# Kernel tuning notes

Measured on AMD Instinct MI355X. Metric: run time of the kernel, lower is better.

## Reference

```python
import jax, jax.numpy as jnp
import numpy as np

GN_EPS = 1e-5
GN_GROUPS = 8
KNN_EPS = 1e-8


def group_norm(x, w, b):
    # x: [B, C, N]
    B, C, N = x.shape
    xg = x.reshape(B, GN_GROUPS, C // GN_GROUPS, N)
    mu = jnp.mean(xg, axis=(2, 3), keepdims=True)
    var = jnp.var(xg, axis=(2, 3), keepdims=True)
    xg = (xg - mu) * jax.lax.rsqrt(var + GN_EPS)
    return xg.reshape(B, C, N) * w[None, :, None] + b[None, :, None]


def swish(x):
    return x * jax.nn.sigmoid(x)


def three_interpolate(points_coords, centers_coords, centers_features):
    # points_coords [B,3,N], centers_coords [B,3,M], centers_features [B,C,M]
    B, _, N = points_coords.shape
    C = centers_features.shape[1]
    p2 = jnp.sum(points_coords ** 2, axis=1)            # [B,N]
    c2 = jnp.sum(centers_coords ** 2, axis=1)           # [B,M]
    cross = jnp.einsum('bdn,bdm->bnm', points_coords, centers_coords)
    dist2 = p2[:, :, None] + c2[:, None, :] - 2.0 * cross  # [B,N,M] squared dists
    neg_d, idx = jax.lax.top_k(-dist2, 3)               # 3 smallest -> [B,N,3]
    d = -neg_d
    w = 1.0 / (d + KNN_EPS)
    w = w / jnp.sum(w, axis=-1, keepdims=True)          # [B,N,3]
    featsT = jnp.swapaxes(centers_features, 1, 2)       # [B,M,C]
    gathered = jnp.take_along_axis(featsT, idx.reshape(B, N * 3, 1), axis=1)
    gathered = gathered.reshape(B, N, 3, C)
    out = jnp.einsum('bnk,bnkc->bcn', w, gathered)      # [B,C,N]
    return out


def setup_inputs() -> dict:
    key = jax.random.key(0)
    ks = jax.random.split(key, 8)
    B, N, M = 8, 8192, 2048
    C_ctr, C_pts, D = 256, 128, 64
    Cin, C1, C2 = C_ctr + C_pts, 256, 256
    return {
        'points_coords': jax.random.normal(ks[0], (B, 3, N), jnp.float32),
        'centers_coords': jax.random.normal(ks[1], (B, 3, M), jnp.float32),
        'centers_features': jax.random.normal(ks[2], (B, C_ctr, M), jnp.float32),
        'points_features': jax.random.normal(ks[3], (B, C_pts, N), jnp.float32),
        'time_emb': jax.random.normal(ks[4], (B, D, 1), jnp.float32),
        'W1': jax.random.normal(ks[5], (C1, Cin), jnp.float32) * (1.0 / np.sqrt(Cin)),
        'b1': jnp.zeros((C1,), jnp.float32),
        'gn1_w': jnp.ones((C1,), jnp.float32),
        'gn1_b': jnp.zeros((C1,), jnp.float32),
        'W2': jax.random.normal(ks[6], (C2, C1), jnp.float32) * (1.0 / np.sqrt(C1)),
        'b2': jnp.zeros((C2,), jnp.float32),
        'gn2_w': jnp.ones((C2,), jnp.float32),
        'gn2_b': jnp.zeros((C2,), jnp.float32),
    }


def reference(points_coords, centers_coords, centers_features, points_features,
              time_emb, W1, b1, gn1_w, gn1_b, W2, b2, gn2_w, gn2_b):
    interp = three_interpolate(points_coords, centers_coords, centers_features)
    x = jnp.concatenate([interp, points_features], axis=1)  # [B, Cin, N]
    # SharedMLP layer 1: Conv1d(k=1) + GroupNorm(8) + Swish
    x = jnp.einsum('oc,bcn->bon', W1, x) + b1[None, :, None]
    x = swish(group_norm(x, gn1_w, gn1_b))
    # layer 2
    x = jnp.einsum('oc,bcn->bon', W2, x) + b2[None, :, None]
    x = swish(group_norm(x, gn2_w, gn2_b))
    N = points_coords.shape[-1]
    time_emb_exp = jnp.broadcast_to(time_emb[:, :, 0:1], time_emb.shape[:2] + (N,))
    return (x, points_coords, time_emb_exp)
```

## Files before the change

### kernel.cpp

```cpp
#include <hip/hip_runtime.h>
#include <hip/hip_bf16.h>
#include <float.h>

#define B_ 8
#define N_ 8192
#define M_ 2048
#define CC_ 256
#define CP_ 128
#define CIN_ 384
#define GRP_ 8

typedef __attribute__((ext_vector_type(8))) short short8;
typedef __attribute__((ext_vector_type(4))) short short4v;
typedef __attribute__((ext_vector_type(4))) float f32x4;

static __device__ __forceinline__ float bf2f(unsigned short u) {
  union { unsigned int i; float f; } v; v.i = ((unsigned int)u) << 16; return v.f;
}
static __device__ __forceinline__ unsigned short f2bf(float f) {
  union { float f; unsigned int i; } v; v.f = f;
  unsigned int u = v.i;
  unsigned int r = (u + 0x7FFFu + ((u >> 16) & 1u)) >> 16;
  return (unsigned short)r;
}
static __device__ __forceinline__ void gload16(const void* g, void* l) {
  __builtin_amdgcn_global_load_lds(
      (const __attribute__((address_space(1))) void*)g,
      (__attribute__((address_space(3))) void*)l, 16, 0, 0);
}

__global__ __launch_bounds__(512) void k_front(
    const float* __restrict__ pc, const float* __restrict__ cc,
    int* __restrict__ idx, float* __restrict__ wts,
    const float* __restrict__ W1, const float* __restrict__ W2,
    short* __restrict__ W1b, short* __restrict__ W2b,
    const float* __restrict__ cf, short* __restrict__ FT,
    const float* __restrict__ pf, short* __restrict__ x0T,
    const float* __restrict__ te, float* __restrict__ out) {
  __shared__ __align__(16) char smem[32768];
  int bid = blockIdx.x;
  int t = threadIdx.x;
  if (bid < 512) {
    float4* ctr = (float4*)smem;
    double (*mk)[3][128] = (double(*)[3][128])smem;
    int b = bid >> 6;
    int base = (bid & 63) * 128;
    const float* ccb = cc + (size_t)b * 3 * M_;
    for (int i = t; i < M_; i += 512) {
      float x = ccb[i], y = ccb[M_ + i], z = ccb[2 * M_ + i];
      ctr[i] = make_float4(x, y, z, x * x + y * y + z * z);
    }
    __syncthreads();
    int wv = t >> 6, lane = t & 63;
    const float* pcb = pc + (size_t)b * 3 * N_;
    int na = base + lane, nb = base + 64 + lane;
    float pxa = pcb[na], pya = pcb[N_ + na], pza = pcb[2 * N_ + na];
    float pxb = pcb[nb], pyb = pcb[N_ + nb], pzb = pcb[2 * N_ + nb];
    float p2a = pxa * pxa + pya * pya + pza * pza;
    float p2b = pxb * pxb + pyb * pyb + pzb * pzb;
    const double kinit = __hiloint2double(0x7F7FFFFF, 0);
    double a0 = kinit, a1 = kinit, a2 = kinit;
    double e0 = kinit, e1 = kinit, e2 = kinit;
    const float4* C = ctr + wv * 256;
    int mbase = wv * 256;
#pragma unroll 8
    for (int m = 0; m < 256; ++m) {
      float4 c = C[m];
      float dota = pxa * c.x;
      dota = __builtin_fmaf(pya, c.y, dota);
      dota = __builtin_fmaf(pza, c.z, dota);
      float da = __builtin_fmaf(-2.f, dota, c.w) + p2a;
      float dotb = pxb * c.x;
      dotb = __builtin_fmaf(pyb, c.y, dotb);
      dotb = __builtin_fmaf(pzb, c.z, dotb);
      float db = __builtin_fmaf(-2.f, dotb, c.w) + p2b;
      double ka = __hiloint2double(__float_as_int(da), mbase + m);
      double kb = __hiloint2double(__float_as_int(db), mbase + m);
      double t0 = fmin(ka, a0);
      double t1 = fmin(fmax(ka, a0), a1);
      double t2 = fmin(fmax(ka, a1), a2);
      a0 = t0; a1 = t1; a2 = t2;
      double u0 = fmin(kb, e0);
      double u1 = fmin(fmax(kb, e0), e1);
      double u2 = fmin(fmax(kb, e1), e2);
      e0 = u0; e1 = u1; e2 = u2;
    }
    __syncthreads();
    mk[wv][0][lane] = a0; mk[wv][1][lane] = a1; mk[wv][2][lane] = a2;
    mk[wv][0][64 + lane] = e0; mk[wv][1][64 + lane] = e1; mk[wv][2][64 + lane] = e2;
    __syncthreads();
    if (t < 128) {
      double k0 = kinit, k1 = kinit, k2 = kinit;
#pragma unroll
      for (int w = 0; w < 8; ++w) {
#pragma unroll
        for (int j = 0; j < 3; ++j) {
          double key = mk[w][j][t];
          double n0 = fmin(key, k0);
          double n1 = fmin(fmax(key, k0), k1);
          double n2 = fmin(fmax(key, k1), k2);
          k0 = n0; k1 = n1; k2 = n2;
        }
      }
      float d0 = __int_as_float(__double2hiint(k0));
      float d1 = __int_as_float(__double2hiint(k1));
      float d2 = __int_as_float(__double2hiint(k2));
      float w0 = 1.f / (d0 + 1e-8f), w1 = 1.f / (d1 + 1e-8f), w2 = 1.f / (d2 + 1e-8f);
      float inv = 1.f / (w0 + w1 + w2);
      int bn = b * N_ + base + t;
      wts[bn] = w0 * inv; wts[B_ * N_ + bn] = w1 * inv; wts[2 * B_ * N_ + bn] = w2 * inv;
      idx[bn] = __double2loint(k0);
      idx[B_ * N_ + bn] = __double2loint(k1);
      idx[2 * B_ * N_ + bn] = __double2loint(k2);
    }
  } else if (bid < 704) {
    int i = (bid - 512) * 512 + t;
    if (i < 256 * CIN_) W1b[i] = (short)f2bf(W1[i]);
    if (i < 256 * 256)  W2b[i] = (short)f2bf(W2[i]);
  } else if (bid < 6848) {
    int q2 = (bid - 704) * 2 + (t >> 8);
    int tt = t & 255;
    float (*tile)[33] = (float(*)[33])(smem + (t >> 8) * 4352);
    const float* in; short* outp;
    int C, Nn, RS, coff, n0, c0, b;
    if (q2 < 4096) {
      in = cf; outp = FT; C = CC_; Nn = M_; RS = CC_; coff = 0;
      n0 = (q2 & 63) * 32; c0 = ((q2 >> 6) & 7) * 32; b = q2 >> 9;
    } else {
      int q = q2 - 4096;
      in = pf; outp = x0T; C = CP_; Nn = N_; RS = CIN_; coff = 256;
      n0 = (q & 255) * 32; c0 = ((q >> 8) & 3) * 32; b = q >> 10;
    }
    const float* inb = in + (size_t)b * C * Nn;
    short* outb = outp + (size_t)b * Nn * RS;
    int tx = tt & 31, ty = tt >> 5;
#pragma unroll
    for (int i = 0; i < 32; i += 8)
      tile[ty + i][tx] = inb[(size_t)(c0 + ty + i) * Nn + n0 + tx];
    __syncthreads();
#pragma unroll
    for (int i = 0; i < 32; i += 8)
      outb[(size_t)(n0 + ty + i) * RS + coff + c0 + tx] = (short)f2bf(tile[tx][ty + i]);
  } else {
    int total = 196608 + B_ * 64 * N_;
    for (int i = (bid - 6848) * 512 + t; i < total; i += 512 * 512) {
      if (i < 196608) {
        out[16777216 + i] = pc[i];
      } else {
        int j = i - 196608;
        int bd = j >> 13;
        out[16973824 + j] = te[bd];
      }
    }
  }
}

__global__ __launch_bounds__(256) void k_interp(
    const short* __restrict__ FT, const int* __restrict__ idx,
    const float* __restrict__ wts, short* __restrict__ x0T) {
  int b = blockIdx.y;
  int t = threadIdx.x;
  int nl = t >> 5, cch = (t & 31) * 8;
  int n = blockIdx.x * 8 + nl;
  int bn = b * N_ + n;
  int i0 = idx[bn], i1 = idx[B_ * N_ + bn], i2 = idx[2 * B_ * N_ + bn];
  float w0 = wts[bn], w1 = wts[B_ * N_ + bn], w2 = wts[2 * B_ * N_ + bn];
  const short* Fb = FT + (size_t)b * M_ * CC_;
  short8 f0 = *(const short8*)(Fb + (size_t)i0 * CC_ + cch);
  short8 f1 = *(const short8*)(Fb + (size_t)i1 * CC_ + cch);
  short8 f2 = *(const short8*)(Fb + (size_t)i2 * CC_ + cch);
  short8 r;
#pragma unroll
  for (int e = 0; e < 8; ++e) {
    float v = w0 * bf2f((unsigned short)f0[e]) + w1 * bf2f((unsigned short)f1[e]) +
              w2 * bf2f((unsigned short)f2[e]);
    r[e] = (short)f2bf(v);
  }
  *(short8*)(x0T + (size_t)bn * CIN_ + cch) = r;
}

__global__ __launch_bounds__(256) void k_gemm(
    const short* __restrict__ Wb, const short* __restrict__ Xb,
    const float* __restrict__ bias, short* __restrict__ Yb,
    float* __restrict__ part, int K) {
  __shared__ __align__(16) short sW[128 * 64];
  __shared__ __align__(16) short sX[128 * 64];
  int b = blockIdx.z;
  int otile = blockIdx.x * 128;
  int ntile = blockIdx.y * 128;
  int t = threadIdx.x;
  int wv = t >> 6, lane = t & 63;
  int wr = wv >> 1, wc = wv & 1;
  int fr = lane & 15;
  int g = lane >> 4;
  f32x4 acc[4][4] = {};
  const short* Wp = Wb + (size_t)otile * K;
  const short* Xp = Xb + ((size_t)b * N_ + ntile) * K;
  for (int k0 = 0; k0 < K; k0 += 64) {
#pragma unroll
    for (int j = 0; j < 4; ++j) {
      int s = j * 256 + t;
      int row = s >> 3;
      int kc = (s & 7) ^ (row & 7);
      gload16(Wp + (size_t)row * K + k0 + kc * 8, sW + j * 2048 + wv * 512);
      gload16(Xp + (size_t)row * K + k0 + kc * 8, sX + j * 2048 + wv * 512);
    }
    __syncthreads();
#pragma unroll
    for (int h = 0; h < 2; ++h) {
      short8 af[4], bfr[4];
#pragma unroll
      for (int m = 0; m < 4; ++m) {
        int ra = wr * 64 + m * 16 + fr;
        af[m] = *(const short8*)(sW + ra * 64 + (((h * 4 + g) ^ (ra & 7)) << 3));
        int rb = wc * 64 + m * 16 + fr;
        bfr[m] = *(const short8*)(sX + rb * 64 + (((h * 4 + g) ^ (rb & 7)) << 3));
      }
#pragma unroll
      for (int m = 0; m < 4; ++m)
#pragma unroll
        for (int nn = 0; nn < 4; ++nn)
          acc[m][nn] = __builtin_amdgcn_mfma_f32_16x16x32_bf16(af[m], bfr[nn], acc[m][nn], 0, 0, 0);
    }
    __syncthreads();
  }
  float s01 = 0.f, ss01 = 0.f, s23 = 0.f, ss23 = 0.f;
#pragma unroll
  for (int m = 0; m < 4; ++m) {
    int o = otile + wr * 64 + m * 16 + g * 4;
    float4 bi = *(const float4*)(bias + o);
#pragma unroll
    for (int nn = 0; nn < 4; ++nn) {
      int n = ntile + wc * 64 + nn * 16 + fr;
      float v0 = acc[m][nn][0] + bi.x;
      float v1 = acc[m][nn][1] + bi.y;
      float v2 = acc[m][nn][2] + bi.z;
      float v3 = acc[m][nn][3] + bi.w;
      if (m < 2) { s01 += v0 + v1 + v2 + v3; ss01 += v0*v0 + v1*v1 + v2*v2 + v3*v3; }
      else       { s23 += v0 + v1 + v2 + v3; ss23 += v0*v0 + v1*v1 + v2*v2 + v3*v3; }
      short4v sv;
      sv[0] = (short)f2bf(v0);
      sv[1] = (short)f2bf(v1);
      sv[2] = (short)f2bf(v2);
      sv[3] = (short)f2bf(v3);
      *(short4v*)(Yb + ((size_t)b * N_ + n) * 256 + o) = sv;
    }
  }
#pragma unroll
  for (int off = 32; off > 0; off >>= 1) {
    s01 += __shfl_down(s01, off);
    ss01 += __shfl_down(ss01, off);
    s23 += __shfl_down(s23, off);
    ss23 += __shfl_down(ss23, off);
  }
  float* wred = (float*)sW;
  if (lane == 0) {
    wred[wv * 4 + 0] = s01; wred[wv * 4 + 1] = ss01;
    wred[wv * 4 + 2] = s23; wred[wv * 4 + 3] = ss23;
  }
  __syncthreads();
  if (t < 8) {
    int gl = t >> 1, sel = t & 1;
    int wrn = gl >> 1;
    int id = (gl & 1) * 2 + sel;
    float v = wred[(wrn * 2 + 0) * 4 + id] + wred[(wrn * 2 + 1) * 4 + id];
    part[(((size_t)b * 8 + blockIdx.x * 4 + gl) * 64 + blockIdx.y) * 2 + sel] = v;
  }
}

__global__ __launch_bounds__(256) void k_gnapply(short* __restrict__ Y,
                                                 const float* __restrict__ part,
                                                 const float* __restrict__ gw,
                                                 const float* __restrict__ gb) {
  __shared__ float fs[128];
  int t = threadIdx.x;
  if (t < 64) {
    float s = 0.f, ss = 0.f;
    for (int j = 0; j < 64; ++j) {
      s += part[((size_t)t * 64 + j) * 2];
      ss += part[((size_t)t * 64 + j) * 2 + 1];
    }
    const float cnt = 32.f * 8192.f;
    float mean = s / cnt;
    float var = ss / cnt - mean * mean;
    fs[t * 2] = mean;
    fs[t * 2 + 1] = rsqrtf(var + 1e-5f);
  }
  __syncthreads();
  unsigned int* Yd = (unsigned int*)Y;
  int total = B_ * N_ * 128;
  for (int i = blockIdx.x * blockDim.x + t; i < total;
       i += gridDim.x * blockDim.x) {
    int o2 = i & 127;
    int b = i >> 20;
    int g = o2 >> 4;
    float mean = fs[(b * 8 + g) * 2], rstd = fs[(b * 8 + g) * 2 + 1];
    unsigned int v = Yd[i];
    int o = o2 * 2;
    float a = bf2f((unsigned short)(v & 0xFFFF));
    float c = bf2f((unsigned short)(v >> 16));
    a = (a - mean) * rstd * gw[o] + gb[o];
    c = (c - mean) * rstd * gw[o + 1] + gb[o + 1];
    a = a / (1.f + __expf(-a));
    c = c / (1.f + __expf(-c));
    Yd[i] = (unsigned int)f2bf(a) | ((unsigned int)f2bf(c) << 16);
  }
}

__global__ __launch_bounds__(256) void k_gnapply_out(
    const short* __restrict__ Y, const float* __restrict__ part,
    const float* __restrict__ gw, const float* __restrict__ gb,
    float* __restrict__ out) {
  __shared__ float tile[64][65];
  __shared__ float fs[16];
  int b = blockIdx.z;
  int t = threadIdx.x;
  if (t < 8) {
    float s = 0.f, ss = 0.f;
    for (int j = 0; j < 64; ++j) {
      s += part[(((size_t)b * 8 + t) * 64 + j) * 2];
      ss += part[(((size_t)b * 8 + t) * 64 + j) * 2 + 1];
    }
    const float cnt = 32.f * 8192.f;
    float mean = s / cnt;
    float var = ss / cnt - mean * mean;
    fs[t * 2] = mean;
    fs[t * 2 + 1] = rsqrtf(var + 1e-5f);
  }
  __syncthreads();
  int n0 = blockIdx.x * 64, o0 = blockIdx.y * 64;
  int row = t >> 5, dcol = t & 31;
  const unsigned int* Yd = (const unsigned int*)(Y + (size_t)b * N_ * 256);
  int o = o0 + dcol * 2;
  int g = o >> 5;
  float mean = fs[g * 2], rstd = fs[g * 2 + 1];
  float w0 = gw[o], w1 = gw[o + 1], bb0 = gb[o], bb1 = gb[o + 1];
#pragma unroll
  for (int p = 0; p < 8; ++p) {
    int n = n0 + p * 8 + row;
    unsigned int v = Yd[(size_t)n * 128 + (o0 >> 1) + dcol];
    float a = bf2f((unsigned short)(v & 0xFFFF));
    float c = bf2f((unsigned short)(v >> 16));
    a = (a - mean) * rstd * w0 + bb0; a = a / (1.f + __expf(-a));
    c = (c - mean) * rstd * w1 + bb1; c = c / (1.f + __expf(-c));
    tile[p * 8 + row][dcol * 2] = a;
    tile[p * 8 + row][dcol * 2 + 1] = c;
  }
  __syncthreads();
  int ol = t >> 2, nch = (t & 3) * 16;
  float* ob = out + ((size_t)(b * 256 + o0 + ol)) * N_ + n0 + nch;
#pragma unroll
  for (int c4 = 0; c4 < 16; c4 += 4) {
    float4 v4;
    v4.x = tile[nch + c4 + 0][ol];
    v4.y = tile[nch + c4 + 1][ol];
    v4.z = tile[nch + c4 + 2][ol];
    v4.w = tile[nch + c4 + 3][ol];
    *(float4*)(ob + c4) = v4;
  }
}

extern "C" void kernel_launch(void* const* d_in, const int* in_sizes, int n_in,
                              void* d_out, int out_size, void* d_ws, size_t ws_size,
                              hipStream_t stream) {
  const float* pc  = (const float*)d_in[0];
  const float* cc  = (const float*)d_in[1];
  const float* cf  = (const float*)d_in[2];
  const float* pf  = (const float*)d_in[3];
  const float* te  = (const float*)d_in[4];
  const float* W1  = (const float*)d_in[5];
  const float* b1  = (const float*)d_in[6];
  const float* g1w = (const float*)d_in[7];
  const float* g1b = (const float*)d_in[8];
  const float* W2  = (const float*)d_in[9];
  const float* b2  = (const float*)d_in[10];
  const float* g2w = (const float*)d_in[11];
  const float* g2b = (const float*)d_in[12];
  float* out = (float*)d_out;

  char* ws = (char*)d_ws;
  size_t off = 0;
  auto alloc = [&](size_t bytes) {
    char* p = ws + off;
    off += (bytes + 255) & ~(size_t)255;
    return p;
  };
  short* FT   = (short*)alloc((size_t)B_ * M_ * CC_ * 2);
  short* x0T  = (short*)alloc((size_t)B_ * N_ * CIN_ * 2);
  short* y1   = (short*)alloc((size_t)B_ * N_ * 256 * 2);
  short* W1b  = (short*)alloc(256 * 384 * 2);
  short* W2b  = (short*)alloc(256 * 256 * 2);
  int*   idx  = (int*)alloc((size_t)3 * B_ * N_ * 4);
  float* wts  = (float*)alloc((size_t)3 * B_ * N_ * 4);
  float* part1 = (float*)alloc(8 * 8 * 64 * 2 * 4);
  float* part2 = (float*)alloc(8 * 8 * 64 * 2 * 4);
  short* y2 = (short*)x0T;

  k_front<<<7360, 512, 0, stream>>>(pc, cc, idx, wts, W1, W2, W1b, W2b,
                                    cf, FT, pf, x0T, te, out);
  k_interp<<<dim3(N_ / 8, B_), 256, 0, stream>>>(FT, idx, wts, x0T);
  k_gemm<<<dim3(2, N_ / 128, B_), 256, 0, stream>>>(W1b, x0T, b1, y1, part1, CIN_);
  k_gnapply<<<2048, 256, 0, stream>>>(y1, part1, g1w, g1b);
  k_gemm<<<dim3(2, N_ / 128, B_), 256, 0, stream>>>(W2b, y1, b2, y2, part2, 256);
  k_gnapply_out<<<dim3(N_ / 64, 4, B_), 256, 0, stream>>>(y2, part2, g2w, g2b, out);
}
```

Baseline: 186.1 us.

## Apply W1 to center features before interpolation and gather projected rows in GEMM epilogue

Because the first 1x1 conv is linear, the interpolation is commuted with it. W1's center-feature columns are applied to the 2048 centers per batch rather than to 8192 interpolated points, and the three-neighbour weighted gather of the projected 256-channel rows moves into the epilogue of the points-feature GEMM. The separate interpolation kernel goes away and the main GEMM's K drops from 384 to 128. In exchange there is a small extra GEMM over the centers, plus scattered gathers of bf16 rows in the epilogue, and the projected features are rounded to bf16 before interpolation.

```diff
diff --git a/kernel.cpp b/kernel.cpp
--- a/kernel.cpp
+++ b/kernel.cpp
@@ -9,6 +9,7 @@
 #define CP_ 128
 #define CIN_ 384
 #define GRP_ 8
+#define BN_ (B_ * N_)
 
 typedef __attribute__((ext_vector_type(8))) short short8;
 typedef __attribute__((ext_vector_type(4))) short short4v;
@@ -108,10 +109,10 @@
       float w0 = 1.f / (d0 + 1e-8f), w1 = 1.f / (d1 + 1e-8f), w2 = 1.f / (d2 + 1e-8f);
       float inv = 1.f / (w0 + w1 + w2);
       int bn = b * N_ + base + t;
-      wts[bn] = w0 * inv; wts[B_ * N_ + bn] = w1 * inv; wts[2 * B_ * N_ + bn] = w2 * inv;
+      wts[bn] = w0 * inv; wts[BN_ + bn] = w1 * inv; wts[2 * BN_ + bn] = w2 * inv;
       idx[bn] = __double2loint(k0);
-      idx[B_ * N_ + bn] = __double2loint(k1);
-      idx[2 * B_ * N_ + bn] = __double2loint(k2);
+      idx[BN_ + bn] = __double2loint(k1);
+      idx[2 * BN_ + bn] = __double2loint(k2);
     }
   } else if (bid < 704) {
     int i = (bid - 512) * 512 + t;
@@ -128,7 +129,7 @@
       n0 = (q2 & 63) * 32; c0 = ((q2 >> 6) & 7) * 32; b = q2 >> 9;
     } else {
       int q = q2 - 4096;
-      in = pf; outp = x0T; C = CP_; Nn = N_; RS = CIN_; coff = 256;
+      in = pf; outp = x0T; C = CP_; Nn = N_; RS = CP_; coff = 0;
       n0 = (q & 255) * 32; c0 = ((q >> 8) & 3) * 32; b = q >> 10;
     }
     const float* inb = in + (size_t)b * C * Nn;
@@ -155,34 +156,14 @@
   }
 }
 
-__global__ __launch_bounds__(256) void k_interp(
-    const short* __restrict__ FT, const int* __restrict__ idx,
-    const float* __restrict__ wts, short* __restrict__ x0T) {
-  int b = blockIdx.y;
-  int t = threadIdx.x;
-  int nl = t >> 5, cch = (t & 31) * 8;
-  int n = blockIdx.x * 8 + nl;
-  int bn = b * N_ + n;
-  int i0 = idx[bn], i1 = idx[B_ * N_ + bn], i2 = idx[2 * B_ * N_ + bn];
-  float w0 = wts[bn], w1 = wts[B_ * N_ + bn], w2 = wts[2 * B_ * N_ + bn];
-  const short* Fb = FT + (size_t)b * M_ * CC_;
-  short8 f0 = *(const short8*)(Fb + (size_t)i0 * CC_ + cch);
-  short8 f1 = *(const short8*)(Fb + (size_t)i1 * CC_ + cch);
-  short8 f2 = *(const short8*)(Fb + (size_t)i2 * CC_ + cch);
-  short8 r;
-#pragma unroll
-  for (int e = 0; e < 8; ++e) {
-    float v = w0 * bf2f((unsigned short)f0[e]) + w1 * bf2f((unsigned short)f1[e]) +
-              w2 * bf2f((unsigned short)f2[e]);
-    r[e] = (short)f2bf(v);
-  }
-  *(short8*)(x0T + (size_t)bn * CIN_ + cch) = r;
-}
-
+template <int MODE>
 __global__ __launch_bounds__(256) void k_gemm(
-    const short* __restrict__ Wb, const short* __restrict__ Xb,
+    const short* __restrict__ Wb, int ldw,
+    const short* __restrict__ Xb, int nrows,
     const float* __restrict__ bias, short* __restrict__ Yb,
-    float* __restrict__ part, int K) {
+    float* __restrict__ part, int K,
+    const short* __restrict__ G, const int* __restrict__ idx,
+    const float* __restrict__ wts) {
   __shared__ __align__(16) short sW[128 * 64];
   __shared__ __align__(16) short sX[128 * 64];
   int b = blockIdx.z;
@@ -194,15 +175,15 @@
   int fr = lane & 15;
   int g = lane >> 4;
   f32x4 acc[4][4] = {};
-  const short* Wp = Wb + (size_t)otile * K;
-  const short* Xp = Xb + ((size_t)b * N_ + ntile) * K;
+  const short* Wp = Wb + (size_t)otile * ldw;
+  const short* Xp = Xb + ((size_t)b * nrows + ntile) * K;
   for (int k0 = 0; k0 < K; k0 += 64) {
 #pragma unroll
     for (int j = 0; j < 4; ++j) {
       int s = j * 256 + t;
       int row = s >> 3;
       int kc = (s & 7) ^ (row & 7);
-      gload16(Wp + (size_t)row * K + k0 + kc * 8, sW + j * 2048 + wv * 512);
+      gload16(Wp + (size_t)row * ldw + k0 + kc * 8, sW + j * 2048 + wv * 512);
       gload16(Xp + (size_t)row * K + k0 + kc * 8, sX + j * 2048 + wv * 512);
     }
     __syncthreads();
@@ -224,11 +205,23 @@
     }
     __syncthreads();
   }
+  int ib0[4], ib1[4], ib2[4];
+  float wt0[4], wt1[4], wt2[4];
+  if constexpr (MODE == 2) {
+#pragma unroll
+    for (int nn = 0; nn < 4; ++nn) {
+      int n = ntile + wc * 64 + nn * 16 + fr;
+      int bn = b * N_ + n;
+      ib0[nn] = idx[bn]; ib1[nn] = idx[BN_ + bn]; ib2[nn] = idx[2 * BN_ + bn];
+      wt0[nn] = wts[bn]; wt1[nn] = wts[BN_ + bn]; wt2[nn] = wts[2 * BN_ + bn];
+    }
+  }
   float s01 = 0.f, ss01 = 0.f, s23 = 0.f, ss23 = 0.f;
 #pragma unroll
   for (int m = 0; m < 4; ++m) {
     int o = otile + wr * 64 + m * 16 + g * 4;
-    float4 bi = *(const float4*)(bias + o);
+    float4 bi = make_float4(0.f, 0.f, 0.f, 0.f);
+    if constexpr (MODE != 0) bi = *(const float4*)(bias + o);
 #pragma unroll
     for (int nn = 0; nn < 4; ++nn) {
       int n = ntile + wc * 64 + nn * 16 + fr;
@@ -236,35 +229,49 @@
       float v1 = acc[m][nn][1] + bi.y;
       float v2 = acc[m][nn][2] + bi.z;
       float v3 = acc[m][nn][3] + bi.w;
-      if (m < 2) { s01 += v0 + v1 + v2 + v3; ss01 += v0*v0 + v1*v1 + v2*v2 + v3*v3; }
-      else       { s23 += v0 + v1 + v2 + v3; ss23 += v0*v0 + v1*v1 + v2*v2 + v3*v3; }
+      if constexpr (MODE == 2) {
+        const short* Gb = G + (size_t)b * M_ * 256 + o;
+        short4v g0 = *(const short4v*)(Gb + (size_t)ib0[nn] * 256);
+        short4v g1 = *(const short4v*)(Gb + (size_t)ib1[nn] * 256);
+        short4v g2 = *(const short4v*)(Gb + (size_t)ib2[nn] * 256);
+        v0 += wt0[nn] * bf2f((unsigned short)g0[0]) + wt1[nn] * bf2f((unsigned short)g1[0]) + wt2[nn] * bf2f((unsigned short)g2[0]);
+        v1 += wt0[nn] * bf2f((unsigned short)g0[1]) + wt1[nn] * bf2f((unsigned short)g1[1]) + wt2[nn] * bf2f((unsigned short)g2[1]);
+        v2 += wt0[nn] * bf2f((unsigned short)g0[2]) + wt1[nn] * bf2f((unsigned short)g1[2]) + wt2[nn] * bf2f((unsigned short)g2[2]);
+        v3 += wt0[nn] * bf2f((unsigned short)g0[3]) + wt1[nn] * bf2f((unsigned short)g1[3]) + wt2[nn] * bf2f((unsigned short)g2[3]);
+      }
+      if constexpr (MODE != 0) {
+        if (m < 2) { s01 += v0 + v1 + v2 + v3; ss01 += v0*v0 + v1*v1 + v2*v2 + v3*v3; }
+        else       { s23 += v0 + v1 + v2 + v3; ss23 += v0*v0 + v1*v1 + v2*v2 + v3*v3; }
+      }
       short4v sv;
       sv[0] = (short)f2bf(v0);
       sv[1] = (short)f2bf(v1);
       sv[2] = (short)f2bf(v2);
       sv[3] = (short)f2bf(v3);
-      *(short4v*)(Yb + ((size_t)b * N_ + n) * 256 + o) = sv;
-    }
-  }
-#pragma unroll
-  for (int off = 32; off > 0; off >>= 1) {
-    s01 += __shfl_down(s01, off);
-    ss01 += __shfl_down(ss01, off);
-    s23 += __shfl_down(s23, off);
-    ss23 += __shfl_down(ss23, off);
-  }
-  float* wred = (float*)sW;
-  if (lane == 0) {
-    wred[wv * 4 + 0] = s01; wred[wv * 4 + 1] = ss01;
-    wred[wv * 4 + 2] = s23; wred[wv * 4 + 3] = ss23;
-  }
-  __syncthreads();
-  if (t < 8) {
-    int gl = t >> 1, sel = t & 1;
-    int wrn = gl >> 1;
-    int id = (gl & 1) * 2 + sel;
-    float v = wred[(wrn * 2 + 0) * 4 + id] + wred[(wrn * 2 + 1) * 4 + id];
-    part[(((size_t)b * 8 + blockIdx.x * 4 + gl) * 64 + blockIdx.y) * 2 + sel] = v;
+      *(short4v*)(Yb + ((size_t)b * nrows + n) * 256 + o) = sv;
+    }
+  }
+  if constexpr (MODE != 0) {
+#pragma unroll
+    for (int off = 32; off > 0; off >>= 1) {
+      s01 += __shfl_down(s01, off);
+      ss01 += __shfl_down(ss01, off);
+      s23 += __shfl_down(s23, off);
+      ss23 += __shfl_down(ss23, off);
+    }
+    float* wred = (float*)sW;
+    if (lane == 0) {
+      wred[wv * 4 + 0] = s01; wred[wv * 4 + 1] = ss01;
+      wred[wv * 4 + 2] = s23; wred[wv * 4 + 3] = ss23;
+    }
+    __syncthreads();
+    if (t < 8) {
+      int gl = t >> 1, sel = t & 1;
+      int wrn = gl >> 1;
+      int id = (gl & 1) * 2 + sel;
+      float v = wred[(wrn * 2 + 0) * 4 + id] + wred[(wrn * 2 + 1) * 4 + id];
+      part[(((size_t)b * 8 + blockIdx.x * 4 + gl) * 64 + blockIdx.y) * 2 + sel] = v;
+    }
   }
 }
 
@@ -379,28 +386,32 @@
   float* out = (float*)d_out;
 
   char* ws = (char*)d_ws;
-  size_t off = 0;
+  short* FT  = (short*)ws;
+  short* G   = (short*)(ws + 8388608);
+  short* x0T = (short*)(ws + 16777216);
+  short* y2  = (short*)ws;
+  size_t off = 33554432;
   auto alloc = [&](size_t bytes) {
     char* p = ws + off;
     off += (bytes + 255) & ~(size_t)255;
     return p;
   };
-  short* FT   = (short*)alloc((size_t)B_ * M_ * CC_ * 2);
-  short* x0T  = (short*)alloc((size_t)B_ * N_ * CIN_ * 2);
   short* y1   = (short*)alloc((size_t)B_ * N_ * 256 * 2);
   short* W1b  = (short*)alloc(256 * 384 * 2);
   short* W2b  = (short*)alloc(256 * 256 * 2);
-  int*   idx  = (int*)alloc((size_t)3 * B_ * N_ * 4);
-  float* wts  = (float*)alloc((size_t)3 * B_ * N_ * 4);
+  int*   idx  = (int*)alloc((size_t)3 * BN_ * 4);
+  float* wts  = (float*)alloc((size_t)3 * BN_ * 4);
   float* part1 = (float*)alloc(8 * 8 * 64 * 2 * 4);
   float* part2 = (float*)alloc(8 * 8 * 64 * 2 * 4);
-  short* y2 = (short*)x0T;
 
   k_front<<<7360, 512, 0, stream>>>(pc, cc, idx, wts, W1, W2, W1b, W2b,
                                     cf, FT, pf, x0T, te, out);
-  k_interp<<<dim3(N_ / 8, B_), 256, 0, stream>>>(FT, idx, wts, x0T);
-  k_gemm<<<dim3(2, N_ / 128, B_), 256, 0, stream>>>(W1b, x0T, b1, y1, part1, CIN_);
+  k_gemm<0><<<dim3(2, M_ / 128, B_), 256, 0, stream>>>(
+      W1b, CIN_, FT, M_, nullptr, G, nullptr, 256, nullptr, nullptr, nullptr);
+  k_gemm<2><<<dim3(2, N_ / 128, B_), 256, 0, stream>>>(
+      W1b + 256, CIN_, x0T, N_, b1, y1, part1, CP_, G, idx, wts);
   k_gnapply<<<2048, 256, 0, stream>>>(y1, part1, g1w, g1b);
-  k_gemm<<<dim3(2, N_ / 128, B_), 256, 0, stream>>>(W2b, y1, b2, y2, part2, 256);
+  k_gemm<1><<<dim3(2, N_ / 128, B_), 256, 0, stream>>>(
+      W2b, 256, y1, N_, b2, y2, part2, 256, nullptr, nullptr, nullptr);
   k_gnapply_out<<<dim3(N_ / 64, 4, B_), 256, 0, stream>>>(y2, part2, g2w, g2b, out);
 }
```

Result: slower. 196.2 us (+5.4%).
